# Optimization experiments

Measured on AMD Instinct MI355X. Metric: run time of the kernel, lower is better.

## Reference

```python
import jax, jax.numpy as jnp
import numpy as np

# Configuration mirroring init_kwargs
B, H, W = 64, 40, 40          # batch, grid (image 1280 / stride 32)
A, C = 5, 80                  # anchors per cell, classes
MAX_BOXES = 100               # max_detection_boxes
SCORE_THR = 0.001             # nms_score_threshold
IOU_THR = 0.5                 # nms_iou_threshold


def setup_inputs() -> dict:
    key = jax.random.key(0)
    k1, k2 = jax.random.split(key)
    predictions = jax.random.normal(k1, (B, H, W, A * (5 + C)), dtype=jnp.float32)
    # anchor (w, h) in grid-cell units, positive
    anchors = jax.random.uniform(k2, (A, 2), dtype=jnp.float32, minval=0.5, maxval=8.0)
    return {"predictions": predictions, "anchors": anchors}


def decode_yolo(predictions, anchors):
    """YOLOv2-style decode -> normalized corner boxes and per-class scores."""
    b, h, w, _ = predictions.shape
    p = predictions.reshape(b, h, w, A, 5 + C)
    gy, gx = jnp.meshgrid(jnp.arange(h, dtype=jnp.float32),
                          jnp.arange(w, dtype=jnp.float32), indexing="ij")
    grid = jnp.stack([gx, gy], axis=-1)[None, :, :, None, :]   # [1,h,w,1,2]
    dims = jnp.array([w, h], dtype=jnp.float32)
    xy = (jax.nn.sigmoid(p[..., 0:2]) + grid) / dims           # normalized centers
    wh = jnp.exp(p[..., 2:4]) * anchors / dims                 # normalized sizes
    conf = jax.nn.sigmoid(p[..., 4:5])
    probs = jax.nn.softmax(p[..., 5:], axis=-1)
    scores = conf * probs                                      # [b,h,w,A,C]
    boxes = jnp.concatenate([xy - wh * 0.5, xy + wh * 0.5], axis=-1)  # x1,y1,x2,y2
    return boxes.reshape(b, -1, 4), scores.reshape(b, -1, C)


def nms_single(boxes, scores_all):
    """Greedy per-class NMS for one image. boxes [N,4], scores_all [N,C]."""
    cls_scores = jnp.max(scores_all, axis=-1)
    classes = jnp.argmax(scores_all, axis=-1)
    s0 = jnp.where(cls_scores > SCORE_THR, cls_scores, -1.0)
    area = jnp.maximum(boxes[:, 2] - boxes[:, 0], 0.0) * \
           jnp.maximum(boxes[:, 3] - boxes[:, 1], 0.0)

    def step(s, _):
        idx = jnp.argmax(s)
        sc = s[idx]
        box = boxes[idx]
        x1 = jnp.maximum(box[0], boxes[:, 0]); y1 = jnp.maximum(box[1], boxes[:, 1])
        x2 = jnp.minimum(box[2], boxes[:, 2]); y2 = jnp.minimum(box[3], boxes[:, 3])
        inter = jnp.maximum(x2 - x1, 0.0) * jnp.maximum(y2 - y1, 0.0)
        box_area = jnp.maximum(box[2] - box[0], 0.0) * jnp.maximum(box[3] - box[1], 0.0)
        iou = inter / (area + box_area - inter + 1e-8)
        suppress = (iou > IOU_THR) & (classes == classes[idx])
        s_new = jnp.where(suppress, -1.0, s).at[idx].set(-1.0)
        valid = sc > 0.0
        out_box = jnp.where(valid, box, 0.0)
        out_sc = jnp.where(valid, sc, 0.0)
        out_cl = jnp.where(valid, classes[idx], -1)
        return s_new, (out_box, out_sc, out_cl)

    _, (ob, osc, ocl) = jax.lax.scan(step, s0, None, length=MAX_BOXES)
    return ob, osc, ocl  # [MAX_BOXES,4], [MAX_BOXES], [MAX_BOXES]


def reference(predictions, anchors):
    boxes, scores = decode_yolo(predictions, anchors)
    sel_boxes, sel_scores, sel_classes = jax.vmap(nms_single)(boxes, scores)
    return sel_boxes, sel_scores, sel_classes
```

## Files before the change

kernel.cpp:

```cpp
#include <hip/hip_runtime.h>
#include <math.h>

#define B 64
#define H 40
#define W 40
#define A 5
#define C 80
#define NBOX (H*W*A)
#define FEAT (5+C)
#define MAXB 100
#define SCORE_THR 0.001f
#define IOU_THR 0.5f

#define DEC_BOXES 64
#define DEC_THREADS 64

#define HBINS 10240
#define BINBASE 119808
#define TARGET 512

#define BK 48
#define RCAP 1024

typedef unsigned long long u64;
typedef unsigned int u32;

__global__ __launch_bounds__(DEC_THREADS) void decode_kernel(
    const float* __restrict__ pred, const float* __restrict__ anchors,
    float* __restrict__ boxes_ws, float* __restrict__ s_ws, int* __restrict__ cls_ws,
    int* __restrict__ ghist)
{
    __shared__ float lds[DEC_BOXES * FEAT];
    const int blk = blockIdx.x;
    const int tid = threadIdx.x;
    const int base_box = blk * DEC_BOXES;

    const float4* src = (const float4*)(pred + (long long)base_box * FEAT);
    float4* dst = (float4*)lds;
    const int n4 = DEC_BOXES * FEAT / 4;
    for (int i = tid; i < n4; i += DEC_THREADS) dst[i] = src[i];
    __syncthreads();

    const int box = base_box + tid;
    const float* l = lds + tid * FEAT;

    int img  = box / NBOX;
    int n    = box - img * NBOX;
    int cell = n / A;
    int a    = n - cell * A;
    int gx   = cell % W;
    int gy   = cell / W;

    float tx = l[0], ty = l[1], tw = l[2], th = l[3], tc = l[4];

    float lg[C];
    #pragma unroll
    for (int i = 0; i < C; ++i) lg[i] = l[5+i];

    float sx = 1.f / (1.f + expf(-tx));
    float sy = 1.f / (1.f + expf(-ty));
    float cx = (sx + (float)gx) / (float)W;
    float cy = (sy + (float)gy) / (float)H;
    float aw = anchors[a*2+0], ah = anchors[a*2+1];
    float bw = expf(tw) * aw / (float)W;
    float bh = expf(th) * ah / (float)H;
    float conf = 1.f / (1.f + expf(-tc));

    float mm[8];
    #pragma unroll
    for (int w = 0; w < 8; ++w) mm[w] = lg[w];
    #pragma unroll
    for (int i = 8; i < C; ++i) mm[i & 7] = fmaxf(mm[i & 7], lg[i]);
    float m = fmaxf(fmaxf(fmaxf(mm[0],mm[1]),fmaxf(mm[2],mm[3])),
                    fmaxf(fmaxf(mm[4],mm[5]),fmaxf(mm[6],mm[7])));

    float sum = 0.f;
    float bv[4] = {-1.f,-1.f,-1.f,-1.f};
    int   bi[4] = {0,0,0,0};
    #pragma unroll
    for (int i = 0; i < C; ++i) {
        float e = expf(lg[i] - m);
        sum += e;
        int w = i & 3;
        if (e > bv[w]) { bv[w] = e; bi[w] = i; }
    }
    float best_e = bv[0]; int best_c = bi[0];
    #pragma unroll
    for (int w = 1; w < 4; ++w) {
        if (bv[w] > best_e || (bv[w] == best_e && bi[w] < best_c)) { best_e = bv[w]; best_c = bi[w]; }
    }

    float score = conf * (best_e / sum);
    float s0 = (score > SCORE_THR) ? score : -1.0f;

    float x1 = cx - bw*0.5f, y1 = cy - bh*0.5f;
    float x2 = cx + bw*0.5f, y2 = cy + bh*0.5f;

    ((float4*)boxes_ws)[box] = make_float4(x1, y1, x2, y2);
    s_ws[box] = s0;
    cls_ws[box] = best_c;

    if (s0 > 0.f) {
        int b = (int)(__float_as_uint(s0) >> 13) - BINBASE;
        b = max(0, min(HBINS-1, b));
        atomicAdd(&ghist[img*HBINS + b], 1);
    }
}

__global__ __launch_bounds__(1024) void scan_kernel(
    const int* __restrict__ ghist, int* __restrict__ tbin, int* __restrict__ bucketCnt)
{
    __shared__ int wavesum[16];
    __shared__ int tbin_s;
    const int img  = blockIdx.x;
    const int tid  = threadIdx.x;
    const int lane = tid & 63;
    const int wid  = tid >> 6;
    const int* gh = ghist + img * HBINS;

    if (tid < C)  bucketCnt[img*C + tid] = 0;
    if (tid == 0) tbin_s = 0;
    __syncthreads();

    int sum_r = 0;
    {
        int base = HBINS - 10*(tid+1);
        #pragma unroll
        for (int q = 0; q < 10; ++q) sum_r += gh[base + q];
    }
    int incl = sum_r;
    #pragma unroll
    for (int off = 1; off < 64; off <<= 1) {
        int o = __shfl_up(incl, off);
        if (lane >= off) incl += o;
    }
    if (lane == 63) wavesum[wid] = incl;
    __syncthreads();
    {
        int wbase = 0;
        for (int w = 0; w < wid; ++w) wbase += wavesum[w];
        int excl = wbase + incl - sum_r;
        if (excl < TARGET && excl + sum_r >= TARGET) {
            int cum = excl;
            for (int q = 0; q < 10; ++q) {
                int b = HBINS - 10*tid - 1 - q;
                cum += gh[b];
                if (cum >= TARGET) { tbin_s = b; break; }
            }
        }
    }
    __syncthreads();
    if (tid == 0) tbin[img] = tbin_s;
}

__global__ __launch_bounds__(256) void scatter_kernel(
    const float* __restrict__ boxes_ws, const float* __restrict__ s_ws,
    const int* __restrict__ cls_ws, const int* __restrict__ tbin,
    int* __restrict__ bucketCnt, u64* __restrict__ bucketKey,
    float4* __restrict__ bucketBox)
{
    const int j = blockIdx.x * 256 + threadIdx.x;
    float s = s_ws[j];
    if (s <= 0.f) return;
    int img = j / NBOX;
    int b = (int)(__float_as_uint(s) >> 13) - BINBASE;
    b = max(0, min(HBINS-1, b));
    if (b < tbin[img]) return;
    int n  = j - img * NBOX;
    int c  = cls_ws[j];
    int bb = img*C + c;
    int pos = atomicAdd(&bucketCnt[bb], 1);
    if (pos < BK) {
        u64 key = ((u64)__float_as_uint(s) << 32)
                | ((u64)(NBOX - n) << 19)
                | ((u64)pos << 13) | (u64)c;
        bucketKey[bb*BK + pos] = key;
        bucketBox[bb*BK + pos] = ((const float4*)boxes_ws)[j];
    }
}

__device__ __forceinline__ u64 wave_max_u64(u64 v) {
    #define STAGE(CTRL, RMASK) { \
        u32 lo = (u32)v, hi = (u32)(v >> 32); \
        u32 tlo = (u32)__builtin_amdgcn_update_dpp(0, (int)lo, CTRL, RMASK, 0xf, true); \
        u32 thi = (u32)__builtin_amdgcn_update_dpp(0, (int)hi, CTRL, RMASK, 0xf, true); \
        u64 t = ((u64)thi << 32) | (u64)tlo; \
        if (t > v) v = t; \
    }
    STAGE(0x111, 0xf)
    STAGE(0x112, 0xf)
    STAGE(0x114, 0xf)
    STAGE(0x118, 0xf)
    STAGE(0x142, 0xa)
    STAGE(0x143, 0xc)
    #undef STAGE
    u32 flo = (u32)__builtin_amdgcn_readlane((int)(u32)v, 63);
    u32 fhi = (u32)__builtin_amdgcn_readlane((int)(v >> 32), 63);
    return ((u64)fhi << 32) | (u64)flo;
}

__global__ __launch_bounds__(64) void classnms_kernel(
    const int* __restrict__ bucketCnt, const u64* __restrict__ bucketKey,
    const float4* __restrict__ bucketBox, u64* __restrict__ survOut)
{
    const int img  = blockIdx.y;
    const int bb   = img*C + blockIdx.x;
    const int lane = threadIdx.x;
    const int n = min(bucketCnt[bb], BK);

    u64 key = 0, keep = 0;
    float x1=0.f, y1=0.f, x2=0.f, y2=0.f, ar=0.f;
    if (lane < n) {
        key = bucketKey[bb*BK + lane];
        float4 b4 = bucketBox[bb*BK + lane];
        x1=b4.x; y1=b4.y; x2=b4.z; y2=b4.w;
        ar = fmaxf(x2-x1,0.f)*fmaxf(y2-y1,0.f);
    }

    for (int t = 0; t < BK; ++t) {
        u64 bk = wave_max_u64(key);
        if (bk == 0) break;
        int sl = (int)((bk >> 13) & 63);
        float sx1 = __shfl(x1, sl), sy1 = __shfl(y1, sl);
        float sx2 = __shfl(x2, sl), sy2 = __shfl(y2, sl);
        float sarea = fmaxf(sx2-sx1,0.f)*fmaxf(sy2-sy1,0.f);

        if (lane == sl) {
            keep = key;
            key = 0;
        } else if (key != 0) {
            float ix1 = fmaxf(sx1, x1);
            float iy1 = fmaxf(sy1, y1);
            float ix2 = fminf(sx2, x2);
            float iy2 = fminf(sy2, y2);
            float inter = fmaxf(ix2-ix1,0.f)*fmaxf(iy2-iy1,0.f);
            float iou = inter / (ar + sarea - inter + 1e-8f);
            if (iou > IOU_THR) key = 0;
        }
    }

    if (lane < BK) survOut[bb*BK + lane] = keep;
}

__global__ __launch_bounds__(256) void rank_kernel(
    const u64* __restrict__ survOut, const float4* __restrict__ bucketBox,
    float* __restrict__ out)
{
    __shared__ u64 ckeys[RCAP];
    __shared__ int cnt;
    const int img = blockIdx.x;
    const int tid = threadIdx.x;

    if (tid == 0) cnt = 0;
    __syncthreads();

    for (int i = tid; i < C*BK; i += 256) {
        u64 k = survOut[(long long)img*C*BK + i];
        if (k != 0) {
            int p = atomicAdd(&cnt, 1);
            if (p < RCAP) ckeys[p] = k;
        }
    }
    __syncthreads();
    const int m = min(cnt, RCAP);

    float* out_boxes  = out;
    float* out_scores = out + B*MAXB*4;
    float* out_cls    = out + B*MAXB*5;

    for (int i = tid; i < m; i += 256) {
        u64 mine = ckeys[i];
        int r = 0;
        for (int j = 0; j < m; ++j) r += (ckeys[j] > mine) ? 1 : 0;
        if (r < MAXB) {
            int c   = (int)(mine & 127);
            int pos = (int)((mine >> 13) & 63);
            float4 b4 = bucketBox[((long long)img*C + c)*BK + pos];
            int o = img*MAXB + r;
            out_boxes[o*4+0] = b4.x; out_boxes[o*4+1] = b4.y;
            out_boxes[o*4+2] = b4.z; out_boxes[o*4+3] = b4.w;
            out_scores[o] = __uint_as_float((u32)(mine >> 32));
            out_cls[o]    = (float)c;
        }
    }

    int base = min(m, MAXB);
    for (int r = base + tid; r < MAXB; r += 256) {
        int o = img*MAXB + r;
        out_boxes[o*4+0]=0.f; out_boxes[o*4+1]=0.f;
        out_boxes[o*4+2]=0.f; out_boxes[o*4+3]=0.f;
        out_scores[o]=0.f;
        out_cls[o]=-1.f;
    }
}

extern "C" void kernel_launch(void* const* d_in, const int* in_sizes, int n_in,
                              void* d_out, int out_size, void* d_ws, size_t ws_size,
                              hipStream_t stream) {
    const float* pred    = (const float*)d_in[0];
    const float* anchors = (const float*)d_in[1];
    float* out = (float*)d_out;

    char* p = (char*)d_ws;
    float*  boxes_ws  = (float*)p;              p += (size_t)B*NBOX*4*sizeof(float);
    float*  s_ws      = (float*)p;              p += (size_t)B*NBOX*sizeof(float);
    int*    cls_ws    = (int*)p;                p += (size_t)B*NBOX*sizeof(int);
    int*    bucketCnt = (int*)p;                p += (size_t)B*C*sizeof(int);
    u64*    bucketKey = (u64*)p;                p += (size_t)B*C*BK*sizeof(u64);
    u64*    survOut   = (u64*)p;                p += (size_t)B*C*BK*sizeof(u64);
    float4* bucketBox = (float4*)p;             p += (size_t)B*C*BK*sizeof(float4);
    int*    ghist     = (int*)p;                p += (size_t)B*HBINS*sizeof(int);
    int*    tbin      = (int*)p;

    hipMemsetAsync(ghist, 0, (size_t)B*HBINS*sizeof(int), stream);
    decode_kernel<<<(B*NBOX)/DEC_BOXES, DEC_THREADS, 0, stream>>>(
        pred, anchors, boxes_ws, s_ws, cls_ws, ghist);
    scan_kernel<<<B, 1024, 0, stream>>>(ghist, tbin, bucketCnt);
    scatter_kernel<<<(B*NBOX)/256, 256, 0, stream>>>(
        boxes_ws, s_ws, cls_ws, tbin, bucketCnt, bucketKey, bucketBox);
    classnms_kernel<<<dim3(C, B), 64, 0, stream>>>(
        bucketCnt, bucketKey, bucketBox, survOut);
    rank_kernel<<<B, 256, 0, stream>>>(
        survOut, bucketBox, out);
}
```

Baseline: 341.7 us.

## Stream decode logits through small padded LDS chunks in two passes

The decode kernel no longer stages a whole 64-box block (about 21KB of LDS) or holds all 80 logits in registers. It now streams each 128-box block through a 16-column, bank-padded LDS tile in six chunks, computing the max in a first pass and re-reading global memory for the exp/sum/argmax pass. This cuts LDS and register use to raise occupancy (launch bounds ask for 6 blocks), at the cost of reading the prediction tensor twice, uncoalesced scalar loads, and many extra barriers.

```diff
diff --git a/kernel.cpp b/kernel.cpp
--- a/kernel.cpp
+++ b/kernel.cpp
@@ -12,8 +12,10 @@
 #define SCORE_THR 0.001f
 #define IOU_THR 0.5f
 
-#define DEC_BOXES 64
-#define DEC_THREADS 64
+#define DEC_BOXES 128
+#define DEC_THREADS 128
+#define CH 16
+#define STRIDE 17
 
 #define HBINS 10240
 #define BINBASE 119808
@@ -25,24 +27,93 @@
 typedef unsigned long long u64;
 typedef unsigned int u32;
 
-__global__ __launch_bounds__(DEC_THREADS) void decode_kernel(
+__global__ __launch_bounds__(DEC_THREADS, 6) void decode_kernel(
     const float* __restrict__ pred, const float* __restrict__ anchors,
     float* __restrict__ boxes_ws, float* __restrict__ s_ws, int* __restrict__ cls_ws,
     int* __restrict__ ghist)
 {
-    __shared__ float lds[DEC_BOXES * FEAT];
-    const int blk = blockIdx.x;
+    __shared__ float st[DEC_BOXES * STRIDE];
     const int tid = threadIdx.x;
-    const int base_box = blk * DEC_BOXES;
-
-    const float4* src = (const float4*)(pred + (long long)base_box * FEAT);
-    float4* dst = (float4*)lds;
-    const int n4 = DEC_BOXES * FEAT / 4;
-    for (int i = tid; i < n4; i += DEC_THREADS) dst[i] = src[i];
-    __syncthreads();
-
+    const int base_box = blockIdx.x * DEC_BOXES;
     const int box = base_box + tid;
-    const float* l = lds + tid * FEAT;
+    const long long rowbase = (long long)base_box * FEAT;
+    const long long LIMIT = (long long)B * NBOX * FEAT - 1;
+
+    auto stage = [&](int c) {
+        #pragma unroll
+        for (int s = 0; s < 16; ++s) {
+            int d  = tid + s * DEC_THREADS;
+            int bi = d >> 4;
+            int k  = d & 15;
+            long long g = rowbase + (long long)bi * FEAT + c*CH + k;
+            if (g > LIMIT) g = LIMIT;
+            st[bi * STRIDE + k] = pred[g];
+        }
+    };
+    const float* row = st + tid * STRIDE;
+
+    float hdr[5];
+    float mm[8];
+    stage(0); __syncthreads();
+    #pragma unroll
+    for (int j = 0; j < 5; ++j) hdr[j] = row[j];
+    #pragma unroll
+    for (int j = 5; j < 13; ++j) mm[j-5] = row[j];
+    #pragma unroll
+    for (int j = 13; j < 16; ++j) {
+        int i = j - 5;
+        mm[i & 7] = fmaxf(mm[i & 7], row[j]);
+    }
+    __syncthreads();
+    #pragma unroll
+    for (int c = 1; c <= 4; ++c) {
+        stage(c); __syncthreads();
+        #pragma unroll
+        for (int j = 0; j < 16; ++j) {
+            int i = c*CH + j - 5;
+            mm[i & 7] = fmaxf(mm[i & 7], row[j]);
+        }
+        __syncthreads();
+    }
+    stage(5); __syncthreads();
+    #pragma unroll
+    for (int j = 0; j < 5; ++j) {
+        int i = 75 + j;
+        mm[i & 7] = fmaxf(mm[i & 7], row[j]);
+    }
+    __syncthreads();
+    float m = fmaxf(fmaxf(fmaxf(mm[0],mm[1]),fmaxf(mm[2],mm[3])),
+                    fmaxf(fmaxf(mm[4],mm[5]),fmaxf(mm[6],mm[7])));
+
+    float sum = 0.f;
+    float bv[4] = {-1.f,-1.f,-1.f,-1.f};
+    int   bi4[4] = {0,0,0,0};
+    #define EXPSTEP(i_, lv_) { \
+        float e = expf((lv_) - m); \
+        sum += e; \
+        if (e > bv[(i_) & 3]) { bv[(i_) & 3] = e; bi4[(i_) & 3] = (i_); } \
+    }
+    stage(0); __syncthreads();
+    #pragma unroll
+    for (int j = 5; j < 16; ++j) { EXPSTEP(j-5, row[j]); }
+    __syncthreads();
+    #pragma unroll
+    for (int c = 1; c <= 4; ++c) {
+        stage(c); __syncthreads();
+        #pragma unroll
+        for (int j = 0; j < 16; ++j) { EXPSTEP(c*CH + j - 5, row[j]); }
+        __syncthreads();
+    }
+    stage(5); __syncthreads();
+    #pragma unroll
+    for (int j = 0; j < 5; ++j) { EXPSTEP(75 + j, row[j]); }
+    #undef EXPSTEP
+
+    float best_e = bv[0]; int best_c = bi4[0];
+    #pragma unroll
+    for (int w = 1; w < 4; ++w) {
+        if (bv[w] > best_e || (bv[w] == best_e && bi4[w] < best_c)) { best_e = bv[w]; best_c = bi4[w]; }
+    }
 
     int img  = box / NBOX;
     int n    = box - img * NBOX;
@@ -51,11 +122,7 @@
     int gx   = cell % W;
     int gy   = cell / W;
 
-    float tx = l[0], ty = l[1], tw = l[2], th = l[3], tc = l[4];
-
-    float lg[C];
-    #pragma unroll
-    for (int i = 0; i < C; ++i) lg[i] = l[5+i];
+    float tx = hdr[0], ty = hdr[1], tw = hdr[2], th = hdr[3], tc = hdr[4];
 
     float sx = 1.f / (1.f + expf(-tx));
     float sy = 1.f / (1.f + expf(-ty));
@@ -65,30 +132,6 @@
     float bw = expf(tw) * aw / (float)W;
     float bh = expf(th) * ah / (float)H;
     float conf = 1.f / (1.f + expf(-tc));
-
-    float mm[8];
-    #pragma unroll
-    for (int w = 0; w < 8; ++w) mm[w] = lg[w];
-    #pragma unroll
-    for (int i = 8; i < C; ++i) mm[i & 7] = fmaxf(mm[i & 7], lg[i]);
-    float m = fmaxf(fmaxf(fmaxf(mm[0],mm[1]),fmaxf(mm[2],mm[3])),
-                    fmaxf(fmaxf(mm[4],mm[5]),fmaxf(mm[6],mm[7])));
-
-    float sum = 0.f;
-    float bv[4] = {-1.f,-1.f,-1.f,-1.f};
-    int   bi[4] = {0,0,0,0};
-    #pragma unroll
-    for (int i = 0; i < C; ++i) {
-        float e = expf(lg[i] - m);
-        sum += e;
-        int w = i & 3;
-        if (e > bv[w]) { bv[w] = e; bi[w] = i; }
-    }
-    float best_e = bv[0]; int best_c = bi[0];
-    #pragma unroll
-    for (int w = 1; w < 4; ++w) {
-        if (bv[w] > best_e || (bv[w] == best_e && bi[w] < best_c)) { best_e = bv[w]; best_c = bi[w]; }
-    }
 
     float score = conf * (best_e / sum);
     float s0 = (score > SCORE_THR) ? score : -1.0f;
```

Result: slower. 617.4 us (+80.7%).

## Fuse scan with scatter and NMS with ranking, load decode input directly to LDS

Applied to the files above, without the earlier changes.

Merges the per-image histogram scan and the candidate scatter into one kernel, and merges the per-class NMS and the final ranking into one 1024-thread kernel per image that keeps survivors in shared memory instead of global memory. The decode kernel now uses direct global-to-LDS loads instead of staging through registers. This removes two kernel launches and a global round trip, at the cost of far fewer blocks (64) for the scatter and NMS phases, each wave serially handling 5 classes.

```diff
diff --git a/kernel.cpp b/kernel.cpp
--- a/kernel.cpp
+++ b/kernel.cpp
@@ -14,6 +14,7 @@
 
 #define DEC_BOXES 64
 #define DEC_THREADS 64
+#define DEC_LDS4 1408
 
 #define HBINS 10240
 #define BINBASE 119808
@@ -30,15 +31,24 @@
     float* __restrict__ boxes_ws, float* __restrict__ s_ws, int* __restrict__ cls_ws,
     int* __restrict__ ghist)
 {
-    __shared__ float lds[DEC_BOXES * FEAT];
-    const int blk = blockIdx.x;
+    __shared__ float lds[DEC_LDS4 * 4];
     const int tid = threadIdx.x;
-    const int base_box = blk * DEC_BOXES;
-
-    const float4* src = (const float4*)(pred + (long long)base_box * FEAT);
-    float4* dst = (float4*)lds;
-    const int n4 = DEC_BOXES * FEAT / 4;
-    for (int i = tid; i < n4; i += DEC_THREADS) dst[i] = src[i];
+    const int base_box = blockIdx.x * DEC_BOXES;
+
+    {
+        const float4* src4 = (const float4*)pred;
+        const long long base4 = (long long)base_box * FEAT / 4;
+        const long long TOT4  = (long long)B * NBOX * FEAT / 4;
+        #pragma unroll
+        for (int i = 0; i < 22; ++i) {
+            long long g4 = base4 + i*64 + tid;
+            if (g4 >= TOT4) g4 = TOT4 - 1;
+            __builtin_amdgcn_global_load_lds(
+                (const __attribute__((address_space(1))) void*)(src4 + g4),
+                (__attribute__((address_space(3))) void*)((char*)lds + i*1024),
+                16, 0, 0);
+        }
+    }
     __syncthreads();
 
     const int box = base_box + tid;
@@ -107,8 +117,12 @@
     }
 }
 
-__global__ __launch_bounds__(1024) void scan_kernel(
-    const int* __restrict__ ghist, int* __restrict__ tbin, int* __restrict__ bucketCnt)
+__global__ __launch_bounds__(1024) void scanscatter_kernel(
+    const int* __restrict__ ghist,
+    const float* __restrict__ boxes_ws, const float* __restrict__ s_ws,
+    const int* __restrict__ cls_ws,
+    int* __restrict__ bucketCnt, u64* __restrict__ bucketKey,
+    float4* __restrict__ bucketBox)
 {
     __shared__ int wavesum[16];
     __shared__ int tbin_s;
@@ -150,32 +164,31 @@
         }
     }
     __syncthreads();
-    if (tid == 0) tbin[img] = tbin_s;
-}
-
-__global__ __launch_bounds__(256) void scatter_kernel(
-    const float* __restrict__ boxes_ws, const float* __restrict__ s_ws,
-    const int* __restrict__ cls_ws, const int* __restrict__ tbin,
-    int* __restrict__ bucketCnt, u64* __restrict__ bucketKey,
-    float4* __restrict__ bucketBox)
-{
-    const int j = blockIdx.x * 256 + threadIdx.x;
-    float s = s_ws[j];
-    if (s <= 0.f) return;
-    int img = j / NBOX;
-    int b = (int)(__float_as_uint(s) >> 13) - BINBASE;
-    b = max(0, min(HBINS-1, b));
-    if (b < tbin[img]) return;
-    int n  = j - img * NBOX;
-    int c  = cls_ws[j];
-    int bb = img*C + c;
-    int pos = atomicAdd(&bucketCnt[bb], 1);
-    if (pos < BK) {
-        u64 key = ((u64)__float_as_uint(s) << 32)
-                | ((u64)(NBOX - n) << 19)
-                | ((u64)pos << 13) | (u64)c;
-        bucketKey[bb*BK + pos] = key;
-        bucketBox[bb*BK + pos] = ((const float4*)boxes_ws)[j];
+    const int tb = tbin_s;
+
+    const long long ib = (long long)img * NBOX;
+    #pragma unroll
+    for (int k = 0; k < 8; ++k) {
+        int n = tid + k*1024;
+        if (n < NBOX) {
+            float s = s_ws[ib + n];
+            if (s > 0.f) {
+                int b = (int)(__float_as_uint(s) >> 13) - BINBASE;
+                b = max(0, min(HBINS-1, b));
+                if (b >= tb) {
+                    int c  = cls_ws[ib + n];
+                    int bb = img*C + c;
+                    int pos = atomicAdd(&bucketCnt[bb], 1);
+                    if (pos < BK) {
+                        u64 key = ((u64)__float_as_uint(s) << 32)
+                                | ((u64)(NBOX - n) << 19)
+                                | ((u64)pos << 13) | (u64)c;
+                        bucketKey[bb*BK + pos] = key;
+                        bucketBox[bb*BK + pos] = ((const float4*)boxes_ws)[ib + n];
+                    }
+                }
+            }
+        }
     }
 }
 
@@ -199,63 +212,62 @@
     return ((u64)fhi << 32) | (u64)flo;
 }
 
-__global__ __launch_bounds__(64) void classnms_kernel(
+__global__ __launch_bounds__(1024) void nmsrank_kernel(
     const int* __restrict__ bucketCnt, const u64* __restrict__ bucketKey,
-    const float4* __restrict__ bucketBox, u64* __restrict__ survOut)
+    const float4* __restrict__ bucketBox, float* __restrict__ out)
 {
-    const int img  = blockIdx.y;
-    const int bb   = img*C + blockIdx.x;
-    const int lane = threadIdx.x;
-    const int n = min(bucketCnt[bb], BK);
-
-    u64 key = 0, keep = 0;
-    float x1=0.f, y1=0.f, x2=0.f, y2=0.f, ar=0.f;
-    if (lane < n) {
-        key = bucketKey[bb*BK + lane];
-        float4 b4 = bucketBox[bb*BK + lane];
-        x1=b4.x; y1=b4.y; x2=b4.z; y2=b4.w;
-        ar = fmaxf(x2-x1,0.f)*fmaxf(y2-y1,0.f);
-    }
-
-    for (int t = 0; t < BK; ++t) {
-        u64 bk = wave_max_u64(key);
-        if (bk == 0) break;
-        int sl = (int)((bk >> 13) & 63);
-        float sx1 = __shfl(x1, sl), sy1 = __shfl(y1, sl);
-        float sx2 = __shfl(x2, sl), sy2 = __shfl(y2, sl);
-        float sarea = fmaxf(sx2-sx1,0.f)*fmaxf(sy2-sy1,0.f);
-
-        if (lane == sl) {
-            keep = key;
-            key = 0;
-        } else if (key != 0) {
-            float ix1 = fmaxf(sx1, x1);
-            float iy1 = fmaxf(sy1, y1);
-            float ix2 = fminf(sx2, x2);
-            float iy2 = fminf(sy2, y2);
-            float inter = fmaxf(ix2-ix1,0.f)*fmaxf(iy2-iy1,0.f);
-            float iou = inter / (ar + sarea - inter + 1e-8f);
-            if (iou > IOU_THR) key = 0;
-        }
-    }
-
-    if (lane < BK) survOut[bb*BK + lane] = keep;
-}
-
-__global__ __launch_bounds__(256) void rank_kernel(
-    const u64* __restrict__ survOut, const float4* __restrict__ bucketBox,
-    float* __restrict__ out)
-{
+    __shared__ u64 skeys[C*BK];
     __shared__ u64 ckeys[RCAP];
     __shared__ int cnt;
-    const int img = blockIdx.x;
-    const int tid = threadIdx.x;
+    const int img  = blockIdx.x;
+    const int tid  = threadIdx.x;
+    const int lane = tid & 63;
+    const int wid  = tid >> 6;
 
     if (tid == 0) cnt = 0;
-    __syncthreads();
-
-    for (int i = tid; i < C*BK; i += 256) {
-        u64 k = survOut[(long long)img*C*BK + i];
+
+    for (int q = 0; q < 5; ++q) {
+        const int c  = wid*5 + q;
+        const int bb = img*C + c;
+        const int n  = min(bucketCnt[bb], BK);
+
+        u64 key = 0, keep = 0;
+        float x1=0.f, y1=0.f, x2=0.f, y2=0.f, ar=0.f;
+        if (lane < n) {
+            key = bucketKey[bb*BK + lane];
+            float4 b4 = bucketBox[bb*BK + lane];
+            x1=b4.x; y1=b4.y; x2=b4.z; y2=b4.w;
+            ar = fmaxf(x2-x1,0.f)*fmaxf(y2-y1,0.f);
+        }
+
+        for (int t = 0; t < BK; ++t) {
+            u64 bk = wave_max_u64(key);
+            if (bk == 0) break;
+            int sl = (int)((bk >> 13) & 63);
+            float sx1 = __shfl(x1, sl), sy1 = __shfl(y1, sl);
+            float sx2 = __shfl(x2, sl), sy2 = __shfl(y2, sl);
+            float sarea = fmaxf(sx2-sx1,0.f)*fmaxf(sy2-sy1,0.f);
+
+            if (lane == sl) {
+                keep = key;
+                key = 0;
+            } else if (key != 0) {
+                float ix1 = fmaxf(sx1, x1);
+                float iy1 = fmaxf(sy1, y1);
+                float ix2 = fminf(sx2, x2);
+                float iy2 = fminf(sy2, y2);
+                float inter = fmaxf(ix2-ix1,0.f)*fmaxf(iy2-iy1,0.f);
+                float iou = inter / (ar + sarea - inter + 1e-8f);
+                if (iou > IOU_THR) key = 0;
+            }
+        }
+
+        if (lane < BK) skeys[c*BK + lane] = keep;
+    }
+    __syncthreads();
+
+    for (int i = tid; i < C*BK; i += 1024) {
+        u64 k = skeys[i];
         if (k != 0) {
             int p = atomicAdd(&cnt, 1);
             if (p < RCAP) ckeys[p] = k;
@@ -268,7 +280,7 @@
     float* out_scores = out + B*MAXB*4;
     float* out_cls    = out + B*MAXB*5;
 
-    for (int i = tid; i < m; i += 256) {
+    for (int i = tid; i < m; i += 1024) {
         u64 mine = ckeys[i];
         int r = 0;
         for (int j = 0; j < m; ++j) r += (ckeys[j] > mine) ? 1 : 0;
@@ -285,7 +297,7 @@
     }
 
     int base = min(m, MAXB);
-    for (int r = base + tid; r < MAXB; r += 256) {
+    for (int r = base + tid; r < MAXB; r += 1024) {
         int o = img*MAXB + r;
         out_boxes[o*4+0]=0.f; out_boxes[o*4+1]=0.f;
         out_boxes[o*4+2]=0.f; out_boxes[o*4+3]=0.f;
@@ -307,19 +319,14 @@
     int*    cls_ws    = (int*)p;                p += (size_t)B*NBOX*sizeof(int);
     int*    bucketCnt = (int*)p;                p += (size_t)B*C*sizeof(int);
     u64*    bucketKey = (u64*)p;                p += (size_t)B*C*BK*sizeof(u64);
-    u64*    survOut   = (u64*)p;                p += (size_t)B*C*BK*sizeof(u64);
     float4* bucketBox = (float4*)p;             p += (size_t)B*C*BK*sizeof(float4);
-    int*    ghist     = (int*)p;                p += (size_t)B*HBINS*sizeof(int);
-    int*    tbin      = (int*)p;
+    int*    ghist     = (int*)p;
 
     hipMemsetAsync(ghist, 0, (size_t)B*HBINS*sizeof(int), stream);
     decode_kernel<<<(B*NBOX)/DEC_BOXES, DEC_THREADS, 0, stream>>>(
         pred, anchors, boxes_ws, s_ws, cls_ws, ghist);
-    scan_kernel<<<B, 1024, 0, stream>>>(ghist, tbin, bucketCnt);
-    scatter_kernel<<<(B*NBOX)/256, 256, 0, stream>>>(
-        boxes_ws, s_ws, cls_ws, tbin, bucketCnt, bucketKey, bucketBox);
-    classnms_kernel<<<dim3(C, B), 64, 0, stream>>>(
-        bucketCnt, bucketKey, bucketBox, survOut);
-    rank_kernel<<<B, 256, 0, stream>>>(
-        survOut, bucketBox, out);
-}
+    scanscatter_kernel<<<B, 1024, 0, stream>>>(
+        ghist, boxes_ws, s_ws, cls_ws, bucketCnt, bucketKey, bucketBox);
+    nmsrank_kernel<<<B, 1024, 0, stream>>>(
+        bucketCnt, bucketKey, bucketBox, out);
+}
```

After: 297.5 us. 12.9% less time.
